# Performance work log

Hardware: AMD Instinct MI355X
Metric: run time of the kernel (lower is better)

Reference implementation:

```python
import jax, jax.numpy as jnp
import numpy as np

DT = 0.001
TAU_MEM = 0.01
TAU_SYN = 0.005
THRESHOLD = 1.0
INITIAL_STATE = 0.0
SS_BETA = 100.0  # SuperSpike surrogate slope (Zenke & Ganguli)


@jax.custom_vjp
def superspike(x):
    # Heaviside spike in forward
    return (x > 0).astype(x.dtype)

def _ss_fwd(x):
    return superspike(x), x

def _ss_bwd(x, g):
    # fast-sigmoid surrogate gradient
    return (g / (SS_BETA * jnp.abs(x) + 1.0) ** 2,)

superspike.defvjp(_ss_fwd, _ss_bwd)


def setup_inputs() -> dict:
    key = jax.random.key(0)
    k1, k2 = jax.random.split(key)
    B, T, IN, OUT = 64, 1024, 256, 256
    inputs = jax.random.normal(k1, (B, T, IN), dtype=jnp.float32)
    w = jax.random.normal(k2, (IN, OUT), dtype=jnp.float32) * 4.0  # scale=4.0 in __init__
    return {"inputs": inputs, "w": w}


def _simulate_mem(inputs, w):
    # inputs: [B, T, IN], w: [IN, OUT]
    x = jnp.matmul(inputs, w)  # [B, T, OUT]
    T = x.shape[1]
    dcy_mem = jnp.exp(jnp.asarray(-DT / (TAU_MEM + 1e-16), dtype=x.dtype))
    scl_mem = 1.0 - dcy_mem
    dcy_syn = jnp.exp(jnp.asarray(-DT / (TAU_SYN + 1e-16), dtype=x.dtype))

    zeros0 = jnp.zeros_like(x[:, 0])  # initial_state = 0

    def step(carry, x_t):
        syn, mem = carry
        new_syn = dcy_syn * syn + x_t
        new_mem = dcy_mem * mem + scl_mem * syn  # uses OLD syn
        out = superspike(mem - THRESHOLD)        # spike from OLD mem
        new_mem = new_mem * (1.0 - out)          # reset
        return (new_syn, new_mem), new_mem

    # loop runs over t = 0 .. T-2 (matches `for t in range(nb_steps - 1)`)
    xs = jnp.swapaxes(x[:, : T - 1], 0, 1)  # [T-1, B, OUT]
    _, mems = jax.lax.scan(step, (zeros0, zeros0), xs)
    mems = jnp.swapaxes(mems, 0, 1)  # [B, T-1, OUT]
    # prepend the initial stored state (zeros, since initial_state=0)
    U = jnp.concatenate([zeros0[:, None, :], mems], axis=1)  # [B, T, OUT]
    return U


def reference(inputs, w):
    # monitor == 'mem' -> return membrane potential trace U
    return _simulate_mem(inputs, w)
```

## Files before the change

### kernel.cpp

```cpp
#include <hip/hip_runtime.h>
#include <cmath>

typedef short bf16x8 __attribute__((ext_vector_type(8)));
typedef float f32x4 __attribute__((ext_vector_type(4)));
typedef unsigned short us8v __attribute__((ext_vector_type(8)));

#define T_DIM 1024

__device__ __forceinline__ unsigned short rtn_bf16(float f) {
    unsigned u = __float_as_uint(f);
    return (unsigned short)((u + 0x7FFFu + ((u >> 16) & 1u)) >> 16);
}
__device__ __forceinline__ float bf_to_f(unsigned short h) {
    return __uint_as_float(((unsigned)h) << 16);
}

__device__ __forceinline__ void split3(float f, unsigned short& h1,
                                       unsigned short& h2, unsigned short& h3) {
    unsigned u = __float_as_uint(f);
    h1 = (unsigned short)(u >> 16);
    float r1 = f - __uint_as_float(u & 0xFFFF0000u);
    unsigned u1 = __float_as_uint(r1);
    h2 = (unsigned short)(u1 >> 16);
    float r2 = r1 - __uint_as_float(u1 & 0xFFFF0000u);
    h3 = rtn_bf16(r2);
}

__global__ __launch_bounds__(256) void lif_wsplit(const float* __restrict__ w,
                                                  unsigned short* __restrict__ wT1,
                                                  unsigned short* __restrict__ wT2,
                                                  unsigned short* __restrict__ wT3) {
    const int id = blockIdx.x * 256 + threadIdx.x;
    const int k = id >> 8, n = id & 255;
    unsigned short h1, h2, h3;
    split3(w[id], h1, h2, h3);
    const int o = n * 256 + k;
    wT1[o] = h1; wT2[o] = h2; wT3[o] = h3;
}

__global__ __launch_bounds__(256) void lif_gemm_mfma(const float* __restrict__ in,
                                                     const unsigned short* __restrict__ wT1,
                                                     const unsigned short* __restrict__ wT2,
                                                     const unsigned short* __restrict__ wT3,
                                                     float* __restrict__ xbuf) {
    __shared__ unsigned short As[3][128 * 64];

    const int tid  = threadIdx.x;
    const int bm   = blockIdx.x;
    const int bn   = blockIdx.y;
    const int wave = tid >> 6;
    const int lane = tid & 63;
    const int l15  = lane & 15;
    const int quad = lane >> 4;
    const int wm   = (wave >> 1) * 64;
    const int wn   = (wave & 1) * 64;

    f32x4 acc[4][4];
    #pragma unroll
    for (int i = 0; i < 4; ++i)
        #pragma unroll
        for (int j = 0; j < 4; ++j) acc[i][j] = (f32x4){0.f, 0.f, 0.f, 0.f};

    const int r  = tid >> 1;
    const int hf = tid & 1;
    const int rx = r & 7;
    const float* arow = in + (size_t)(bm * 128 + r) * 256 + hf * 32;

    for (int kt = 0; kt < 4; ++kt) {
        const int k0 = kt * 64;
        float4 av[8];
        #pragma unroll
        for (int j = 0; j < 8; ++j)
            av[j] = *(const float4*)(arow + k0 + j * 4);

        __syncthreads();
        #pragma unroll
        for (int j2 = 0; j2 < 4; ++j2) {
            const float fv[8] = {av[2*j2].x, av[2*j2].y, av[2*j2].z, av[2*j2].w,
                                 av[2*j2+1].x, av[2*j2+1].y, av[2*j2+1].z, av[2*j2+1].w};
            us8v o1, o2, o3;
            #pragma unroll
            for (int i = 0; i < 8; ++i) {
                unsigned short h1, h2, h3;
                split3(fv[i], h1, h2, h3);
                o1[i] = h1; o2[i] = h2; o3[i] = h3;
            }
            const int cp = ((hf * 4 + j2) ^ rx) * 8;
            *(us8v*)&As[0][r * 64 + cp] = o1;
            *(us8v*)&As[1][r * 64 + cp] = o2;
            *(us8v*)&As[2][r * 64 + cp] = o3;
        }
        __syncthreads();

        #pragma unroll
        for (int ks = 0; ks < 2; ++ks) {
            bf16x8 af[3][4];
            const int ko = ((ks * 4 + quad) ^ (l15 & 7)) * 8;
            #pragma unroll
            for (int mt = 0; mt < 4; ++mt) {
                const int ro = (wm + mt * 16 + l15) * 64 + ko;
                af[0][mt] = *(const bf16x8*)&As[0][ro];
                af[1][mt] = *(const bf16x8*)&As[1][ro];
                af[2][mt] = *(const bf16x8*)&As[2][ro];
            }
            #pragma unroll
            for (int nt = 0; nt < 4; ++nt) {
                const int ncol = bn * 128 + wn + nt * 16 + l15;
                const size_t wo = (size_t)ncol * 256 + k0 + ks * 32 + quad * 8;
                const bf16x8 b1 = *(const bf16x8*)(wT1 + wo);
                const bf16x8 b2 = *(const bf16x8*)(wT2 + wo);
                const bf16x8 b3 = *(const bf16x8*)(wT3 + wo);
                #pragma unroll
                for (int mt = 0; mt < 4; ++mt) {
                    f32x4 a = acc[mt][nt];
                    a = __builtin_amdgcn_mfma_f32_16x16x32_bf16(af[0][mt], b1, a, 0, 0, 0);
                    a = __builtin_amdgcn_mfma_f32_16x16x32_bf16(af[0][mt], b2, a, 0, 0, 0);
                    a = __builtin_amdgcn_mfma_f32_16x16x32_bf16(af[1][mt], b1, a, 0, 0, 0);
                    a = __builtin_amdgcn_mfma_f32_16x16x32_bf16(af[1][mt], b2, a, 0, 0, 0);
                    a = __builtin_amdgcn_mfma_f32_16x16x32_bf16(af[0][mt], b3, a, 0, 0, 0);
                    a = __builtin_amdgcn_mfma_f32_16x16x32_bf16(af[2][mt], b1, a, 0, 0, 0);
                    acc[mt][nt] = a;
                }
            }
        }
    }

    #pragma unroll
    for (int mt = 0; mt < 4; ++mt) {
        #pragma unroll
        for (int nt = 0; nt < 4; ++nt) {
            const int C = bn * 128 + wn + nt * 16 + l15;
            const int Rb = bm * 128 + wm + mt * 16 + quad * 4;
            #pragma unroll
            for (int reg = 0; reg < 4; ++reg)
                xbuf[(size_t)(Rb + reg) * 256 + C] = acc[mt][nt][reg];
        }
    }
}

__global__ __launch_bounds__(64) void lif_scan(const float* __restrict__ xbuf,
                                               float* __restrict__ U,
                                               double dcy_syn, double dcy_mem,
                                               double scl_mem) {
    __shared__ float xs[64][64];

    const int b    = blockIdx.x >> 2;
    const int og   = blockIdx.x & 3;
    const int lane = threadIdx.x;

    const float* src = xbuf + (size_t)b * T_DIM * 256 + og * 64;
    float* up = U + (size_t)b * T_DIM * 256 + og * 64 + lane;

    up[0] = 0.0f;
    double syn = 0.0, mem = 0.0;

    float4 pre[16];
    #pragma unroll
    for (int i = 0; i < 16; ++i) {
        const int f = i * 64 + lane;
        pre[i] = *(const float4*)(src + (size_t)(f >> 4) * 256 + (f & 15) * 4);
    }

    for (int c = 0; c < 16; ++c) {
        __syncthreads();
        #pragma unroll
        for (int i = 0; i < 16; ++i) {
            const int f = i * 64 + lane;
            *(float4*)&xs[f >> 4][(f & 15) * 4] = pre[i];
        }
        __syncthreads();
        if (c < 15) {
            const float* nsrc = src + (size_t)(c + 1) * 64 * 256;
            #pragma unroll
            for (int i = 0; i < 16; ++i) {
                const int f = i * 64 + lane;
                pre[i] = *(const float4*)(nsrc + (size_t)(f >> 4) * 256 + (f & 15) * 4);
            }
        }
        const int tbase = c * 64;
        #pragma unroll 8
        for (int j = 0; j < 64; ++j) {
            const double x = (double)xs[j][lane];
            double nm = dcy_mem * mem + scl_mem * syn;
            if (mem - 1.0 > 0.0) nm = 0.0;
            syn = dcy_syn * syn + x;
            mem = nm;
            const int t = tbase + j;
            if (t < T_DIM - 1)
                up[(size_t)(t + 1) * 256] = (float)mem;
        }
    }
}

extern "C" void kernel_launch(void* const* d_in, const int* in_sizes, int n_in,
                              void* d_out, int out_size, void* d_ws, size_t ws_size,
                              hipStream_t stream) {
    const float* in = (const float*)d_in[0];
    const float* w  = (const float*)d_in[1];
    float* U = (float*)d_out;

    const double dcy_mem = exp(-0.001 / (0.01  + 1e-16));
    const double dcy_syn = exp(-0.001 / (0.005 + 1e-16));
    const double scl_mem = 1.0 - dcy_mem;

    char* ws = (char*)d_ws;
    unsigned short* wT1 = (unsigned short*)ws;
    unsigned short* wT2 = (unsigned short*)(ws + 131072);
    unsigned short* wT3 = (unsigned short*)(ws + 262144);
    float* xbuf = (float*)(ws + 524288);

    lif_wsplit<<<dim3(256), dim3(256), 0, stream>>>(w, wT1, wT2, wT3);
    lif_gemm_mfma<<<dim3(512, 2), dim3(256), 0, stream>>>(in, wT1, wT2, wT3, xbuf);
    lif_scan<<<dim3(256), dim3(64), 0, stream>>>(xbuf, U, dcy_syn, dcy_mem, scl_mem);
}
```

Baseline: 224.4 us.

## Stage W limbs in LDS, split A at fragment load, register-buffer scan inputs

The GEMM now stores the raw fp32 A tile in LDS with an XOR swizzle and does the three-way bf16 split per fragment just before the MFMAs, instead of splitting once and storing three bf16 planes. The three W limbs are cooperatively staged into LDS per k-tile, so they are no longer read straight from global memory by each wave. The scan kernel drops its shared-memory transpose and instead double-buffers per-thread strided loads in registers, using nontemporal loads and stores. The trade-off is redundant split arithmetic, since each A element is now split once per wave that reads it, plus higher LDS use (about 80 KB per block), which may reduce occupancy.

```diff
diff --git a/kernel.cpp b/kernel.cpp
--- a/kernel.cpp
+++ b/kernel.cpp
@@ -3,7 +3,6 @@
 
 typedef short bf16x8 __attribute__((ext_vector_type(8)));
 typedef float f32x4 __attribute__((ext_vector_type(4)));
-typedef unsigned short us8v __attribute__((ext_vector_type(8)));
 
 #define T_DIM 1024
 
@@ -14,7 +13,6 @@
 __device__ __forceinline__ float bf_to_f(unsigned short h) {
     return __uint_as_float(((unsigned)h) << 16);
 }
-
 __device__ __forceinline__ void split3(float f, unsigned short& h1,
                                        unsigned short& h2, unsigned short& h3) {
     unsigned u = __float_as_uint(f);
@@ -43,7 +41,8 @@
                                                      const unsigned short* __restrict__ wT2,
                                                      const unsigned short* __restrict__ wT3,
                                                      float* __restrict__ xbuf) {
-    __shared__ unsigned short As[3][128 * 64];
+    __shared__ float          As[128 * 64];
+    __shared__ unsigned short WL[3 * 128 * 64];
 
     const int tid  = threadIdx.x;
     const int bm   = blockIdx.x;
@@ -63,8 +62,8 @@
 
     const int r  = tid >> 1;
     const int hf = tid & 1;
-    const int rx = r & 7;
     const float* arow = in + (size_t)(bm * 128 + r) * 256 + hf * 32;
+    const unsigned short* wTs[3] = {wT1, wT2, wT3};
 
     for (int kt = 0; kt < 4; ++kt) {
         const int k0 = kt * 64;
@@ -75,41 +74,48 @@
 
         __syncthreads();
         #pragma unroll
-        for (int j2 = 0; j2 < 4; ++j2) {
-            const float fv[8] = {av[2*j2].x, av[2*j2].y, av[2*j2].z, av[2*j2].w,
-                                 av[2*j2+1].x, av[2*j2+1].y, av[2*j2+1].z, av[2*j2+1].w};
-            us8v o1, o2, o3;
-            #pragma unroll
-            for (int i = 0; i < 8; ++i) {
-                unsigned short h1, h2, h3;
-                split3(fv[i], h1, h2, h3);
-                o1[i] = h1; o2[i] = h2; o3[i] = h3;
-            }
-            const int cp = ((hf * 4 + j2) ^ rx) * 8;
-            *(us8v*)&As[0][r * 64 + cp] = o1;
-            *(us8v*)&As[1][r * 64 + cp] = o2;
-            *(us8v*)&As[2][r * 64 + cp] = o3;
+        for (int j = 0; j < 8; ++j) {
+            const int sw = ((hf * 8 + j) ^ (r & 15)) * 4;
+            *(float4*)&As[r * 64 + sw] = av[j];
+        }
+        #pragma unroll
+        for (int j = 0; j < 12; ++j) {
+            const int c    = j * 256 + tid;
+            const int limb = c >> 10;
+            const int rem  = c & 1023;
+            const int nl   = rem >> 3;
+            const int ch   = rem & 7;
+            const unsigned short* src = wTs[limb] + (size_t)(bn * 128 + nl) * 256 + k0 + ch * 8;
+            *(bf16x8*)&WL[limb * 8192 + nl * 64 + ((ch ^ (nl & 7)) * 8)] = *(const bf16x8*)src;
         }
         __syncthreads();
 
         #pragma unroll
         for (int ks = 0; ks < 2; ++ks) {
             bf16x8 af[3][4];
-            const int ko = ((ks * 4 + quad) ^ (l15 & 7)) * 8;
             #pragma unroll
             for (int mt = 0; mt < 4; ++mt) {
-                const int ro = (wm + mt * 16 + l15) * 64 + ko;
-                af[0][mt] = *(const bf16x8*)&As[0][ro];
-                af[1][mt] = *(const bf16x8*)&As[1][ro];
-                af[2][mt] = *(const bf16x8*)&As[2][ro];
+                const int m = wm + mt * 16 + l15;
+                const int cbase = 2 * (ks * 4 + quad);
+                float4 f0 = *(const float4*)&As[m * 64 + ((cbase    ) ^ l15) * 4];
+                float4 f1 = *(const float4*)&As[m * 64 + ((cbase + 1) ^ l15) * 4];
+                const float fv[8] = {f0.x, f0.y, f0.z, f0.w, f1.x, f1.y, f1.z, f1.w};
+                #pragma unroll
+                for (int i = 0; i < 8; ++i) {
+                    unsigned short h1, h2, h3;
+                    split3(fv[i], h1, h2, h3);
+                    af[0][mt][i] = (short)h1;
+                    af[1][mt][i] = (short)h2;
+                    af[2][mt][i] = (short)h3;
+                }
             }
             #pragma unroll
             for (int nt = 0; nt < 4; ++nt) {
-                const int ncol = bn * 128 + wn + nt * 16 + l15;
-                const size_t wo = (size_t)ncol * 256 + k0 + ks * 32 + quad * 8;
-                const bf16x8 b1 = *(const bf16x8*)(wT1 + wo);
-                const bf16x8 b2 = *(const bf16x8*)(wT2 + wo);
-                const bf16x8 b3 = *(const bf16x8*)(wT3 + wo);
+                const int nl = wn + nt * 16 + l15;
+                const int wo = nl * 64 + (((ks * 4 + quad) ^ (nl & 7)) * 8);
+                const bf16x8 b1 = *(const bf16x8*)&WL[          wo];
+                const bf16x8 b2 = *(const bf16x8*)&WL[ 8192 +   wo];
+                const bf16x8 b3 = *(const bf16x8*)&WL[16384 +   wo];
                 #pragma unroll
                 for (int mt = 0; mt < 4; ++mt) {
                     f32x4 a = acc[mt][nt];
@@ -129,7 +135,7 @@
     for (int mt = 0; mt < 4; ++mt) {
         #pragma unroll
         for (int nt = 0; nt < 4; ++nt) {
-            const int C = bn * 128 + wn + nt * 16 + l15;
+            const int C  = bn * 128 + wn + nt * 16 + l15;
             const int Rb = bm * 128 + wm + mt * 16 + quad * 4;
             #pragma unroll
             for (int reg = 0; reg < 4; ++reg)
@@ -142,52 +148,39 @@
                                                float* __restrict__ U,
                                                double dcy_syn, double dcy_mem,
                                                double scl_mem) {
-    __shared__ float xs[64][64];
-
-    const int b    = blockIdx.x >> 2;
-    const int og   = blockIdx.x & 3;
-    const int lane = threadIdx.x;
-
-    const float* src = xbuf + (size_t)b * T_DIM * 256 + og * 64;
-    float* up = U + (size_t)b * T_DIM * 256 + og * 64 + lane;
+    const int b = blockIdx.x >> 2;
+    const int o = (blockIdx.x & 3) * 64 + threadIdx.x;
+
+    const float* xp = xbuf + (size_t)b * T_DIM * 256 + o;
+    float* up = U + (size_t)b * T_DIM * 256 + o;
 
     up[0] = 0.0f;
     double syn = 0.0, mem = 0.0;
 
-    float4 pre[16];
+    float xr[2][32];
     #pragma unroll
-    for (int i = 0; i < 16; ++i) {
-        const int f = i * 64 + lane;
-        pre[i] = *(const float4*)(src + (size_t)(f >> 4) * 256 + (f & 15) * 4);
-    }
-
-    for (int c = 0; c < 16; ++c) {
-        __syncthreads();
-        #pragma unroll
-        for (int i = 0; i < 16; ++i) {
-            const int f = i * 64 + lane;
-            *(float4*)&xs[f >> 4][(f & 15) * 4] = pre[i];
-        }
-        __syncthreads();
-        if (c < 15) {
-            const float* nsrc = src + (size_t)(c + 1) * 64 * 256;
-            #pragma unroll
-            for (int i = 0; i < 16; ++i) {
-                const int f = i * 64 + lane;
-                pre[i] = *(const float4*)(nsrc + (size_t)(f >> 4) * 256 + (f & 15) * 4);
+    for (int j = 0; j < 32; ++j)
+        xr[0][j] = __builtin_nontemporal_load(xp + (size_t)j * 256);
+
+    for (int bt = 0; bt < 32; ++bt) {
+        const int cur = bt & 1;
+        if (bt < 31) {
+            const float* np = xp + (size_t)(bt + 1) * 32 * 256;
+            #pragma unroll
+            for (int j = 0; j < 32; ++j)
+                xr[cur ^ 1][j] = __builtin_nontemporal_load(np + (size_t)j * 256);
+        }
+        const int tb = bt * 32;
+        #pragma unroll
+        for (int j = 0; j < 32; ++j) {
+            const int t = tb + j;
+            if (t < T_DIM - 1) {
+                double nm = dcy_mem * mem + scl_mem * syn;
+                if (mem - 1.0 > 0.0) nm = 0.0;
+                syn = dcy_syn * syn + (double)xr[cur][j];
+                mem = nm;
+                __builtin_nontemporal_store((float)mem, up + (size_t)(t + 1) * 256);
             }
-        }
-        const int tbase = c * 64;
-        #pragma unroll 8
-        for (int j = 0; j < 64; ++j) {
-            const double x = (double)xs[j][lane];
-            double nm = dcy_mem * mem + scl_mem * syn;
-            if (mem - 1.0 > 0.0) nm = 0.0;
-            syn = dcy_syn * syn + x;
-            mem = nm;
-            const int t = tbase + j;
-            if (t < T_DIM - 1)
-                up[(size_t)(t + 1) * 256] = (float)mem;
         }
     }
 }
```

Result: slower. 263.0 us (+17.2%).

## Double-buffer scan inputs in registers and prefetch GEMM B fragments

Applied to the files above, without the earlier changes.

The scan kernel no longer stages x through LDS with block barriers. Each thread instead loads its own column straight into two 32-deep register buffers in ping-pong fashion, and uses nontemporal loads and stores to overlap global latency with the serial recurrence. The GEMM inner loop now software-pipelines the weight fragment loads one n-tile ahead. Both changes raise register pressure, and the scan's per-thread strided scalar loads give up the float4 coalescing the old path had.

```diff
diff --git a/kernel.cpp b/kernel.cpp
--- a/kernel.cpp
+++ b/kernel.cpp
@@ -14,7 +14,6 @@
 __device__ __forceinline__ float bf_to_f(unsigned short h) {
     return __uint_as_float(((unsigned)h) << 16);
 }
-
 __device__ __forceinline__ void split3(float f, unsigned short& h1,
                                        unsigned short& h2, unsigned short& h3) {
     unsigned u = __float_as_uint(f);
@@ -103,13 +102,21 @@
                 af[1][mt] = *(const bf16x8*)&As[1][ro];
                 af[2][mt] = *(const bf16x8*)&As[2][ro];
             }
+
+            size_t wo = (size_t)(bn * 128 + wn + l15) * 256 + k0 + ks * 32 + quad * 8;
+            bf16x8 b1 = *(const bf16x8*)(wT1 + wo);
+            bf16x8 b2 = *(const bf16x8*)(wT2 + wo);
+            bf16x8 b3 = *(const bf16x8*)(wT3 + wo);
+
             #pragma unroll
             for (int nt = 0; nt < 4; ++nt) {
-                const int ncol = bn * 128 + wn + nt * 16 + l15;
-                const size_t wo = (size_t)ncol * 256 + k0 + ks * 32 + quad * 8;
-                const bf16x8 b1 = *(const bf16x8*)(wT1 + wo);
-                const bf16x8 b2 = *(const bf16x8*)(wT2 + wo);
-                const bf16x8 b3 = *(const bf16x8*)(wT3 + wo);
+                bf16x8 n1, n2, n3;
+                if (nt < 3) {
+                    const size_t won = wo + (size_t)16 * 256;
+                    n1 = *(const bf16x8*)(wT1 + won);
+                    n2 = *(const bf16x8*)(wT2 + won);
+                    n3 = *(const bf16x8*)(wT3 + won);
+                }
                 #pragma unroll
                 for (int mt = 0; mt < 4; ++mt) {
                     f32x4 a = acc[mt][nt];
@@ -121,6 +128,7 @@
                     a = __builtin_amdgcn_mfma_f32_16x16x32_bf16(af[2][mt], b1, a, 0, 0, 0);
                     acc[mt][nt] = a;
                 }
+                if (nt < 3) { b1 = n1; b2 = n2; b3 = n3; wo += (size_t)16 * 256; }
             }
         }
     }
@@ -129,7 +137,7 @@
     for (int mt = 0; mt < 4; ++mt) {
         #pragma unroll
         for (int nt = 0; nt < 4; ++nt) {
-            const int C = bn * 128 + wn + nt * 16 + l15;
+            const int C  = bn * 128 + wn + nt * 16 + l15;
             const int Rb = bm * 128 + wm + mt * 16 + quad * 4;
             #pragma unroll
             for (int reg = 0; reg < 4; ++reg)
@@ -142,52 +150,53 @@
                                                float* __restrict__ U,
                                                double dcy_syn, double dcy_mem,
                                                double scl_mem) {
-    __shared__ float xs[64][64];
-
-    const int b    = blockIdx.x >> 2;
-    const int og   = blockIdx.x & 3;
-    const int lane = threadIdx.x;
-
-    const float* src = xbuf + (size_t)b * T_DIM * 256 + og * 64;
-    float* up = U + (size_t)b * T_DIM * 256 + og * 64 + lane;
+    const int b = blockIdx.x >> 2;
+    const int o = (blockIdx.x & 3) * 64 + threadIdx.x;
+
+    const float* xp = xbuf + (size_t)b * T_DIM * 256 + o;
+    float* up = U + (size_t)b * T_DIM * 256 + o;
 
     up[0] = 0.0f;
     double syn = 0.0, mem = 0.0;
 
-    float4 pre[16];
+    float bufA[32], bufB[32];
     #pragma unroll
-    for (int i = 0; i < 16; ++i) {
-        const int f = i * 64 + lane;
-        pre[i] = *(const float4*)(src + (size_t)(f >> 4) * 256 + (f & 15) * 4);
-    }
-
-    for (int c = 0; c < 16; ++c) {
-        __syncthreads();
-        #pragma unroll
-        for (int i = 0; i < 16; ++i) {
-            const int f = i * 64 + lane;
-            *(float4*)&xs[f >> 4][(f & 15) * 4] = pre[i];
-        }
-        __syncthreads();
-        if (c < 15) {
-            const float* nsrc = src + (size_t)(c + 1) * 64 * 256;
-            #pragma unroll
-            for (int i = 0; i < 16; ++i) {
-                const int f = i * 64 + lane;
-                pre[i] = *(const float4*)(nsrc + (size_t)(f >> 4) * 256 + (f & 15) * 4);
-            }
-        }
-        const int tbase = c * 64;
-        #pragma unroll 8
-        for (int j = 0; j < 64; ++j) {
-            const double x = (double)xs[j][lane];
+    for (int j = 0; j < 32; ++j)
+        bufA[j] = __builtin_nontemporal_load(xp + (size_t)j * 256);
+
+    #pragma unroll 1
+    for (int bt = 0; bt < 16; ++bt) {
+        const int tb = bt * 64;
+        {
+            const float* np = xp + (size_t)(tb + 32) * 256;
+            #pragma unroll
+            for (int j = 0; j < 32; ++j)
+                bufB[j] = __builtin_nontemporal_load(np + (size_t)j * 256);
+        }
+        #pragma unroll
+        for (int j = 0; j < 32; ++j) {
+            const int t = tb + j;
             double nm = dcy_mem * mem + scl_mem * syn;
             if (mem - 1.0 > 0.0) nm = 0.0;
-            syn = dcy_syn * syn + x;
+            syn = dcy_syn * syn + (double)bufA[j];
             mem = nm;
-            const int t = tbase + j;
+            __builtin_nontemporal_store((float)mem, up + (size_t)(t + 1) * 256);
+        }
+        if (bt < 15) {
+            const float* np = xp + (size_t)(tb + 64) * 256;
+            #pragma unroll
+            for (int j = 0; j < 32; ++j)
+                bufA[j] = __builtin_nontemporal_load(np + (size_t)j * 256);
+        }
+        #pragma unroll
+        for (int j = 0; j < 32; ++j) {
+            const int t = tb + 32 + j;
+            double nm = dcy_mem * mem + scl_mem * syn;
+            if (mem - 1.0 > 0.0) nm = 0.0;
+            syn = dcy_syn * syn + (double)bufB[j];
+            mem = nm;
             if (t < T_DIM - 1)
-                up[(size_t)(t + 1) * 256] = (float)mem;
+                __builtin_nontemporal_store((float)mem, up + (size_t)(t + 1) * 256);
         }
     }
 }
```

Result: faster. 199.7 us (-11.0%).
